# Optimization experiments

Hardware: AMD Instinct MI355X
Metric: run time of the kernel (lower is better)

## Reference

```python
import jax, jax.numpy as jnp
import numpy as np

ROPE_BASE = 10000.0
NUM_HEADS = 16

def _rotate_half(x):
    d = x.shape[-1] // 2
    return jnp.concatenate([-x[..., d:], x[..., :d]], axis=-1)

def setup_inputs() -> dict:
    key = jax.random.key(0)
    ks = jax.random.split(key, 5)
    b, s, d = 1, 2048, 2048
    scale = 1.0 / np.sqrt(d)
    return {
        "hidden_states": jax.random.normal(ks[0], (b, s, d), jnp.float32),
        "wq": jax.random.normal(ks[1], (d, d), jnp.float32) * scale,
        "wk": jax.random.normal(ks[2], (d, d), jnp.float32) * scale,
        "wv": jax.random.normal(ks[3], (d, d), jnp.float32) * scale,
        "wo": jax.random.normal(ks[4], (d, d), jnp.float32) * scale,
        "position_ids": jnp.broadcast_to(jnp.arange(s, dtype=jnp.int32), (b, s)),
    }

def reference(hidden_states, wq, wk, wv, wo, position_ids):
    b, s, d = hidden_states.shape
    h = NUM_HEADS
    dh = d // h
    # q/k/v projections (torch Linear: y = x @ W^T), split heads -> bhsd
    def proj(w):
        return jnp.einsum('bsd,ed->bse', hidden_states, w).reshape(b, s, h, dh).transpose(0, 2, 1, 3)
    q, k, v = proj(wq), proj(wk), proj(wv)
    # rotary embedding (LLaMA style): freqs over half dim, duplicated
    inv_freq = 1.0 / (ROPE_BASE ** (jnp.arange(0, dh, 2, dtype=jnp.float32) / dh))
    t = jnp.arange(s, dtype=jnp.float32)
    freqs = jnp.einsum('s,f->sf', t, inv_freq)              # [s, dh/2]
    emb = jnp.concatenate([freqs, freqs], axis=-1)          # [s, dh]
    cos = jnp.cos(emb)[position_ids][:, None, :, :]         # [b,1,s,dh]
    sin = jnp.sin(emb)[position_ids][:, None, :, :]
    q = q * cos + _rotate_half(q) * sin
    k = k * cos + _rotate_half(k) * sin
    # full (non-causal) scaled dot-product attention, as in the SDPA fast path
    scores = jnp.einsum('bhqd,bhkd->bhqk', q, k) / jnp.sqrt(jnp.float32(dh))
    attn = jax.nn.softmax(scores, axis=-1)
    out = jnp.einsum('bhqk,bhkd->bhqd', attn, v)            # [b,h,s,dh]
    out = out.transpose(0, 2, 1, 3).reshape(b, s, d)
    return jnp.einsum('bsd,ed->bse', out, wo)
```

## Files before the change

### kernel.cpp

```cpp
#include <hip/hip_runtime.h>

typedef unsigned short ushort_t;
typedef unsigned int uint32;
typedef __attribute__((ext_vector_type(8))) short short8;
typedef __attribute__((ext_vector_type(4))) float f32x4;
typedef __attribute__((ext_vector_type(2))) uint32 u32x2;

#define LDS_LOAD16(gptr, lptr)                                                             \
  __builtin_amdgcn_global_load_lds((const __attribute__((address_space(1))) uint32*)(gptr),\
                                   (__attribute__((address_space(3))) uint32*)(lptr),      \
                                   16, 0, 0)

__device__ __forceinline__ ushort_t f2b(float f) {
  uint32 u = __builtin_bit_cast(uint32, f);
  u += 0x7fffu + ((u >> 16) & 1u);
  return (ushort_t)(u >> 16);
}
__device__ __forceinline__ uint32 pk2(float a, float b) {
  return (uint32)f2b(a) | ((uint32)f2b(b) << 16);
}
__device__ __forceinline__ int swz8(int r) { return (r ^ (r >> 3)) & 7; }

constexpr size_t E = (size_t)2048 * 2048;

__global__ __launch_bounds__(256) void k_cvt5(const float* __restrict__ a0, const float* __restrict__ a1,
                                              const float* __restrict__ a2, const float* __restrict__ a3,
                                              const float* __restrict__ a4, ushort_t* __restrict__ out) {
  const float* srcs[5] = {a0, a1, a2, a3, a4};
  const float* s = srcs[blockIdx.y];
  size_t i = ((size_t)blockIdx.x * 256 + threadIdx.x) * 4;
  float4 v = *(const float4*)(s + i);
  ushort4 o;
  o.x = f2b(v.x); o.y = f2b(v.y); o.z = f2b(v.z); o.w = f2b(v.w);
  *(ushort4*)(out + (size_t)blockIdx.y * E + i) = o;
}

__global__ __launch_bounds__(256) void k_gemm_qkv(const ushort_t* __restrict__ A,
                                                  const ushort_t* __restrict__ B0,
                                                  const ushort_t* __restrict__ B1,
                                                  const ushort_t* __restrict__ B2,
                                                  ushort_t* __restrict__ Qm,
                                                  ushort_t* __restrict__ Km,
                                                  ushort_t* __restrict__ Vt,
                                                  const int* __restrict__ pos) {
  __shared__ ushort_t As[128 * 64];
  __shared__ ushort_t Bs[128 * 64];
  const int tid = threadIdx.x;
  const int lane = tid & 63, wave = tid >> 6;
  const int quad = lane >> 4, l16 = lane & 15;
  const int wm = wave >> 1, wn = wave & 1;
  const int z = blockIdx.z;
  const ushort_t* Bp = (z == 0) ? B0 : (z == 1) ? B1 : B2;
  const size_t row0 = (size_t)blockIdx.y * 128, col0 = (size_t)blockIdx.x * 128;

  int g[4];
#pragma unroll
  for (int j = 0; j < 4; ++j) g[j] = (j & 1) + ((j >> 1) << 2) + wn * 2;

  f32x4 zero = {0.f, 0.f, 0.f, 0.f};
  f32x4 acc[4][4];
#pragma unroll
  for (int i = 0; i < 4; ++i)
#pragma unroll
    for (int j = 0; j < 4; ++j) acc[i][j] = zero;

  for (int kt = 0; kt < 32; ++kt) {
#pragma unroll
    for (int j2 = 0; j2 < 4; ++j2) {
      int c = tid + 256 * j2;
      int r = c >> 3, p = c & 7;
      int sc = (p ^ swz8(r)) * 8;
      LDS_LOAD16(A + (row0 + r) * 2048 + kt * 64 + sc, &As[c * 8]);
      LDS_LOAD16(Bp + (col0 + r) * 2048 + kt * 64 + sc, &Bs[c * 8]);
    }
    __syncthreads();
    short8 a[4][2], b[4][2];
#pragma unroll
    for (int i = 0; i < 4; ++i) {
      int ra = wm * 64 + i * 16 + l16;
#pragma unroll
      for (int kk = 0; kk < 2; ++kk)
        a[i][kk] = *(const short8*)&As[(ra * 8 + ((kk * 4 + quad) ^ swz8(ra))) * 8];
    }
#pragma unroll
    for (int j = 0; j < 4; ++j) {
      int rb = g[j] * 16 + l16;
#pragma unroll
      for (int kk = 0; kk < 2; ++kk)
        b[j][kk] = *(const short8*)&Bs[(rb * 8 + ((kk * 4 + quad) ^ swz8(rb))) * 8];
    }
#pragma unroll
    for (int kk = 0; kk < 2; ++kk)
#pragma unroll
      for (int i = 0; i < 4; ++i)
#pragma unroll
        for (int j = 0; j < 4; ++j)
          acc[i][j] = __builtin_amdgcn_mfma_f32_16x16x32_bf16(a[i][kk], b[j][kk], acc[i][j], 0, 0, 0);
    __syncthreads();
  }

  if (z < 2) {
    ushort_t* C = z ? Km : Qm;
    const float mul = z ? 1.0f : 0.08838834764831845f;
#pragma unroll
    for (int i = 0; i < 4; ++i)
#pragma unroll
      for (int r = 0; r < 4; ++r) {
        size_t row = row0 + wm * 64 + i * 16 + quad * 4 + r;
        float pt = (float)pos[row];
        size_t rowoff = row * 2048 + col0;
#pragma unroll
        for (int j = 0; j < 2; ++j) {
          int f = g[j] * 16 + l16;
          float ang = pt * __expf(-0.14391156831212787f * (float)f);
          float sn, cs;
          __sincosf(ang, &sn, &cs);
          cs *= mul; sn *= mul;
          float q0 = acc[i][j][r], q1 = acc[i][j + 2][r];
          C[rowoff + f]      = f2b(q0 * cs - q1 * sn);
          C[rowoff + f + 64] = f2b(q1 * cs + q0 * sn);
        }
      }
  } else {
#pragma unroll
    for (int i = 0; i < 4; ++i)
#pragma unroll
      for (int j = 0; j < 4; ++j) {
        size_t col = col0 + g[j] * 16 + l16;
        size_t rowb = row0 + wm * 64 + i * 16 + quad * 4;
        ushort4 ov;
        ov.x = f2b(acc[i][j][0]); ov.y = f2b(acc[i][j][1]);
        ov.z = f2b(acc[i][j][2]); ov.w = f2b(acc[i][j][3]);
        *(ushort4*)&Vt[col * 2048 + rowb] = ov;
      }
  }
}

__global__ __launch_bounds__(256, 2) void k_attn(const ushort_t* __restrict__ Q,
                                                 const ushort_t* __restrict__ Kg,
                                                 const ushort_t* __restrict__ Vt,
                                                 ushort_t* __restrict__ O) {
  __shared__ uint32 smem[9216 + 256];
  ushort_t* Qs  = (ushort_t*)smem;
  uint32*   Pbf = smem + 4096;
  float*    Lred = (float*)(smem + 9216);
  float*    Rbuf = (float*)smem;

  const int tid = threadIdx.x;
  const int lane = tid & 63, wave = tid >> 6;
  const int quad = lane >> 4, l16 = lane & 15;
  const int bid = blockIdx.x;
  const int head = ((bid & 7) << 1) + ((bid >> 3) >> 5);
  const int qt = (bid >> 3) & 31;

#pragma unroll
  for (int j = 0; j < 4; ++j) {
    int s = tid + 256 * j;
    int r = s >> 4, p = s & 15;
    LDS_LOAD16(Q + (size_t)(qt * 64 + r) * 2048 + head * 128 + ((p ^ (r & 15)) * 8), &Qs[s * 8]);
  }
  __syncthreads();

  f32x4 zero = {0.f, 0.f, 0.f, 0.f};
  f32x4 oacc[4][8];
#pragma unroll
  for (int qg = 0; qg < 4; ++qg)
#pragma unroll
    for (int ns = 0; ns < 8; ++ns) oacc[qg][ns] = zero;
  float l_acc[4] = {0.f, 0.f, 0.f, 0.f};

  const ushort_t* Kbase = Kg + (size_t)head * 128;
  const ushort_t* Vbase = Vt + (size_t)head * 128 * 2048;
  uint32* pw = Pbf + wave * 1280;

  for (int it = 0; it < 16; ++it) {
    const int kb = it * 128 + wave * 32;

    short8 kf[2][4];
#pragma unroll
    for (int kg = 0; kg < 2; ++kg)
#pragma unroll
      for (int kk = 0; kk < 4; ++kk)
        kf[kg][kk] = *(const short8*)&Kbase[(size_t)(kb + kg * 16 + l16) * 2048 + kk * 32 + quad * 8];

#pragma unroll
    for (int qg = 0; qg < 4; ++qg) {
      short8 qa[4];
#pragma unroll
      for (int kk = 0; kk < 4; ++kk)
        qa[kk] = *(const short8*)&Qs[((qg * 16 + l16) * 16 + ((kk * 4 + quad) ^ l16)) * 8];
      f32x4 s0 = zero, s1 = zero;
#pragma unroll
      for (int kk = 0; kk < 4; ++kk) {
        s0 = __builtin_amdgcn_mfma_f32_16x16x32_bf16(kf[0][kk], qa[kk], s0, 0, 0, 0);
        s1 = __builtin_amdgcn_mfma_f32_16x16x32_bf16(kf[1][kk], qa[kk], s1, 0, 0, 0);
      }
      float p00 = __expf(s0[0]), p01 = __expf(s0[1]);
      float p02 = __expf(s0[2]), p03 = __expf(s0[3]);
      float p10 = __expf(s1[0]), p11 = __expf(s1[1]);
      float p12 = __expf(s1[2]), p13 = __expf(s1[3]);
      l_acc[qg] += ((p00 + p01) + (p02 + p03)) + ((p10 + p11) + (p12 + p13));
      u32x2 w0, w1;
      w0[0] = pk2(p00, p01); w0[1] = pk2(p02, p03);
      w1[0] = pk2(p10, p11); w1[1] = pk2(p12, p13);
      int off = (qg * 16 + l16) * 20 + quad * 2;
      *(u32x2*)&pw[off]     = w0;
      *(u32x2*)&pw[off + 8] = w1;
    }

    short8 pb[4];
#pragma unroll
    for (int qg = 0; qg < 4; ++qg)
      pb[qg] = *(const short8*)&pw[(qg * 16 + l16) * 20 + quad * 4];

#pragma unroll
    for (int ns = 0; ns < 8; ++ns) {
      const short8 vf = *(const short8*)&Vbase[(size_t)(ns * 16 + l16) * 2048 + kb + quad * 8];
#pragma unroll
      for (int qg = 0; qg < 4; ++qg)
        oacc[qg][ns] = __builtin_amdgcn_mfma_f32_16x16x32_bf16(vf, pb[qg], oacc[qg][ns], 0, 0, 0);
    }
  }

#pragma unroll
  for (int qg = 0; qg < 4; ++qg) {
    float l = l_acc[qg];
    l += __shfl_xor(l, 16, 64);
    l += __shfl_xor(l, 32, 64);
    l_acc[qg] = l;
  }
  if (quad == 0) {
#pragma unroll
    for (int qg = 0; qg < 4; ++qg) Lred[wave * 64 + qg * 16 + l16] = l_acc[qg];
  }

  const int tq = tid >> 4;
  const int td = (tid & 15) * 8;
  for (int qg = 0; qg < 4; ++qg) {
    __syncthreads();
#pragma unroll
    for (int ns = 0; ns < 8; ++ns)
      *(f32x4*)&Rbuf[(wave * 16 + l16) * 132 + ns * 16 + quad * 4] = oacc[qg][ns];
    __syncthreads();
    float lt = Lred[qg * 16 + tq] + Lred[64 + qg * 16 + tq] +
               Lred[128 + qg * 16 + tq] + Lred[192 + qg * 16 + tq];
    float inv = 1.0f / lt;
    f32x4 sA = zero, sB = zero;
#pragma unroll
    for (int w = 0; w < 4; ++w) {
      sA += *(const f32x4*)&Rbuf[(w * 16 + tq) * 132 + td];
      sB += *(const f32x4*)&Rbuf[(w * 16 + tq) * 132 + td + 4];
    }
    ushort4 o1, o2;
    o1.x = f2b(sA[0] * inv); o1.y = f2b(sA[1] * inv);
    o1.z = f2b(sA[2] * inv); o1.w = f2b(sA[3] * inv);
    o2.x = f2b(sB[0] * inv); o2.y = f2b(sB[1] * inv);
    o2.z = f2b(sB[2] * inv); o2.w = f2b(sB[3] * inv);
    size_t orow = (size_t)(qt * 64 + qg * 16 + tq) * 2048 + head * 128 + td;
    *(ushort4*)&O[orow] = o1;
    *(ushort4*)&O[orow + 4] = o2;
  }
}

__global__ __launch_bounds__(256) void k_gemm_wo_sk(const ushort_t* __restrict__ A,
                                                    const ushort_t* __restrict__ B,
                                                    float* __restrict__ P) {
  __shared__ ushort_t As[128 * 64];
  __shared__ ushort_t Bs[128 * 64];
  const int tid = threadIdx.x;
  const int lane = tid & 63, wave = tid >> 6;
  const int quad = lane >> 4, l16 = lane & 15;
  const int wm = wave >> 1, wn = wave & 1;
  const size_t row0 = (size_t)blockIdx.y * 128, col0 = (size_t)blockIdx.x * 128;
  const int k0 = blockIdx.z * 1024;
  float* Pz = P + (size_t)blockIdx.z * E;

  f32x4 zero = {0.f, 0.f, 0.f, 0.f};
  f32x4 acc[4][4];
#pragma unroll
  for (int i = 0; i < 4; ++i)
#pragma unroll
    for (int j = 0; j < 4; ++j) acc[i][j] = zero;

  for (int kt = 0; kt < 16; ++kt) {
#pragma unroll
    for (int j2 = 0; j2 < 4; ++j2) {
      int c = tid + 256 * j2;
      int r = c >> 3, p = c & 7;
      int sc = (p ^ swz8(r)) * 8;
      LDS_LOAD16(A + (row0 + r) * 2048 + k0 + kt * 64 + sc, &As[c * 8]);
      LDS_LOAD16(B + (col0 + r) * 2048 + k0 + kt * 64 + sc, &Bs[c * 8]);
    }
    __syncthreads();
    short8 a[4][2], b[4][2];
#pragma unroll
    for (int i = 0; i < 4; ++i) {
      int ra = wm * 64 + i * 16 + l16;
#pragma unroll
      for (int kk = 0; kk < 2; ++kk)
        a[i][kk] = *(const short8*)&As[(ra * 8 + ((kk * 4 + quad) ^ swz8(ra))) * 8];
    }
#pragma unroll
    for (int j = 0; j < 4; ++j) {
      int rb = wn * 64 + j * 16 + l16;
#pragma unroll
      for (int kk = 0; kk < 2; ++kk)
        b[j][kk] = *(const short8*)&Bs[(rb * 8 + ((kk * 4 + quad) ^ swz8(rb))) * 8];
    }
#pragma unroll
    for (int kk = 0; kk < 2; ++kk)
#pragma unroll
      for (int i = 0; i < 4; ++i)
#pragma unroll
        for (int j = 0; j < 4; ++j)
          acc[i][j] = __builtin_amdgcn_mfma_f32_16x16x32_bf16(a[i][kk], b[j][kk], acc[i][j], 0, 0, 0);
    __syncthreads();
  }

#pragma unroll
  for (int i = 0; i < 4; ++i)
#pragma unroll
    for (int j = 0; j < 4; ++j)
#pragma unroll
      for (int r = 0; r < 4; ++r) {
        size_t row = row0 + wm * 64 + i * 16 + quad * 4 + r;
        size_t col = col0 + wn * 64 + j * 16 + l16;
        Pz[row * 2048 + col] = acc[i][j][r];
      }
}

__global__ __launch_bounds__(256) void k_red(const float* __restrict__ P, float* __restrict__ out) {
  size_t i = ((size_t)blockIdx.x * 256 + threadIdx.x) * 4;
  f32x4 a = *(const f32x4*)(P + i);
  f32x4 b = *(const f32x4*)(P + E + i);
  *(f32x4*)(out + i) = a + b;
}

extern "C" void kernel_launch(void* const* d_in, const int* in_sizes, int n_in,
                              void* d_out, int out_size, void* d_ws, size_t ws_size,
                              hipStream_t stream) {
  const float* X  = (const float*)d_in[0];
  const float* wq = (const float*)d_in[1];
  const float* wk = (const float*)d_in[2];
  const float* wv = (const float*)d_in[3];
  const float* wo = (const float*)d_in[4];
  const int*  pos = (const int*)d_in[5];
  float* out = (float*)d_out;

  if (ws_size < 9 * E * sizeof(ushort_t)) return;

  ushort_t* Xb  = (ushort_t*)d_ws;
  ushort_t* Wqb = Xb + E;
  ushort_t* Wkb = Xb + 2 * E;
  ushort_t* Wvb = Xb + 3 * E;
  ushort_t* Wob = Xb + 4 * E;
  ushort_t* Qm  = Xb + 5 * E;
  ushort_t* Km  = Xb + 6 * E;
  ushort_t* Vtm = Xb + 7 * E;
  ushort_t* Om  = Xb + 8 * E;
  float* Pf = (float*)Xb;

  dim3 b256(256);
  k_cvt5<<<dim3(4096, 5), b256, 0, stream>>>(X, wq, wk, wv, wo, Xb);
  k_gemm_qkv<<<dim3(16, 16, 3), b256, 0, stream>>>(Xb, Wqb, Wkb, Wvb, Qm, Km, Vtm, pos);
  k_attn<<<512, b256, 0, stream>>>(Qm, Km, Vtm, Om);
  k_gemm_wo_sk<<<dim3(16, 16, 2), b256, 0, stream>>>(Om, Wob, Pf);
  k_red<<<4096, b256, 0, stream>>>(Pf, out);
}
```

Before: 317.7 us.

## Halve attention query tile to 32 rows, doubling blocks and raising occupancy

The attention kernel now processes 32 query rows per block instead of 64 and launches 1024 blocks instead of 512. Per-wave accumulators shrink from 4x8 to 2x8 MFMA tiles, and the LDS buffers are split and resized, which allows a launch bound of 3 blocks per SM. The aim is better CU fill and occupancy on a 256-CU part for latency hiding. In exchange, each K/V tile is reused across half as many queries, doubling total K/V global/L2 traffic, and the epilogue takes more barrier rounds.

```diff
diff --git a/kernel.cpp b/kernel.cpp
--- a/kernel.cpp
+++ b/kernel.cpp
@@ -136,42 +136,41 @@
   }
 }
 
-__global__ __launch_bounds__(256, 2) void k_attn(const ushort_t* __restrict__ Q,
+__global__ __launch_bounds__(256, 3) void k_attn(const ushort_t* __restrict__ Q,
                                                  const ushort_t* __restrict__ Kg,
                                                  const ushort_t* __restrict__ Vt,
                                                  ushort_t* __restrict__ O) {
-  __shared__ uint32 smem[9216 + 256];
-  ushort_t* Qs  = (ushort_t*)smem;
-  uint32*   Pbf = smem + 4096;
-  float*    Lred = (float*)(smem + 9216);
-  float*    Rbuf = (float*)smem;
+  __shared__ ushort_t Qs[32 * 128];
+  __shared__ uint32 Pbf[4 * 32 * 20];
+  __shared__ float Rbuf[4 * 16 * 68];
+  __shared__ float Lred[4][2][16];
 
   const int tid = threadIdx.x;
   const int lane = tid & 63, wave = tid >> 6;
   const int quad = lane >> 4, l16 = lane & 15;
   const int bid = blockIdx.x;
-  const int head = ((bid & 7) << 1) + ((bid >> 3) >> 5);
-  const int qt = (bid >> 3) & 31;
-
-#pragma unroll
-  for (int j = 0; j < 4; ++j) {
+  const int head = ((bid & 7) << 1) | (bid >> 9);
+  const int qt = (bid >> 3) & 63;
+
+#pragma unroll
+  for (int j = 0; j < 2; ++j) {
     int s = tid + 256 * j;
     int r = s >> 4, p = s & 15;
-    LDS_LOAD16(Q + (size_t)(qt * 64 + r) * 2048 + head * 128 + ((p ^ (r & 15)) * 8), &Qs[s * 8]);
+    LDS_LOAD16(Q + (size_t)(qt * 32 + r) * 2048 + head * 128 + ((p ^ (r & 15)) * 8), &Qs[s * 8]);
   }
   __syncthreads();
 
   f32x4 zero = {0.f, 0.f, 0.f, 0.f};
-  f32x4 oacc[4][8];
-#pragma unroll
-  for (int qg = 0; qg < 4; ++qg)
+  f32x4 oacc[2][8];
+#pragma unroll
+  for (int qg = 0; qg < 2; ++qg)
 #pragma unroll
     for (int ns = 0; ns < 8; ++ns) oacc[qg][ns] = zero;
-  float l_acc[4] = {0.f, 0.f, 0.f, 0.f};
+  float l_acc[2] = {0.f, 0.f};
 
   const ushort_t* Kbase = Kg + (size_t)head * 128;
   const ushort_t* Vbase = Vt + (size_t)head * 128 * 2048;
-  uint32* pw = Pbf + wave * 1280;
+  uint32* pw = Pbf + wave * 640;
 
   for (int it = 0; it < 16; ++it) {
     const int kb = it * 128 + wave * 32;
@@ -184,7 +183,7 @@
         kf[kg][kk] = *(const short8*)&Kbase[(size_t)(kb + kg * 16 + l16) * 2048 + kk * 32 + quad * 8];
 
 #pragma unroll
-    for (int qg = 0; qg < 4; ++qg) {
+    for (int qg = 0; qg < 2; ++qg) {
       short8 qa[4];
 #pragma unroll
       for (int kk = 0; kk < 4; ++kk)
@@ -208,58 +207,50 @@
       *(u32x2*)&pw[off + 8] = w1;
     }
 
-    short8 pb[4];
-#pragma unroll
-    for (int qg = 0; qg < 4; ++qg)
+    short8 pb[2];
+#pragma unroll
+    for (int qg = 0; qg < 2; ++qg)
       pb[qg] = *(const short8*)&pw[(qg * 16 + l16) * 20 + quad * 4];
 
 #pragma unroll
     for (int ns = 0; ns < 8; ++ns) {
       const short8 vf = *(const short8*)&Vbase[(size_t)(ns * 16 + l16) * 2048 + kb + quad * 8];
 #pragma unroll
-      for (int qg = 0; qg < 4; ++qg)
+      for (int qg = 0; qg < 2; ++qg)
         oacc[qg][ns] = __builtin_amdgcn_mfma_f32_16x16x32_bf16(vf, pb[qg], oacc[qg][ns], 0, 0, 0);
     }
   }
 
 #pragma unroll
-  for (int qg = 0; qg < 4; ++qg) {
+  for (int qg = 0; qg < 2; ++qg) {
     float l = l_acc[qg];
     l += __shfl_xor(l, 16, 64);
     l += __shfl_xor(l, 32, 64);
-    l_acc[qg] = l;
-  }
-  if (quad == 0) {
-#pragma unroll
-    for (int qg = 0; qg < 4; ++qg) Lred[wave * 64 + qg * 16 + l16] = l_acc[qg];
+    if (quad == 0) Lred[wave][qg][l16] = l;
   }
 
   const int tq = tid >> 4;
-  const int td = (tid & 15) * 8;
-  for (int qg = 0; qg < 4; ++qg) {
-    __syncthreads();
-#pragma unroll
-    for (int ns = 0; ns < 8; ++ns)
-      *(f32x4*)&Rbuf[(wave * 16 + l16) * 132 + ns * 16 + quad * 4] = oacc[qg][ns];
-    __syncthreads();
-    float lt = Lred[qg * 16 + tq] + Lred[64 + qg * 16 + tq] +
-               Lred[128 + qg * 16 + tq] + Lred[192 + qg * 16 + tq];
-    float inv = 1.0f / lt;
-    f32x4 sA = zero, sB = zero;
-#pragma unroll
-    for (int w = 0; w < 4; ++w) {
-      sA += *(const f32x4*)&Rbuf[(w * 16 + tq) * 132 + td];
-      sB += *(const f32x4*)&Rbuf[(w * 16 + tq) * 132 + td + 4];
-    }
-    ushort4 o1, o2;
-    o1.x = f2b(sA[0] * inv); o1.y = f2b(sA[1] * inv);
-    o1.z = f2b(sA[2] * inv); o1.w = f2b(sA[3] * inv);
-    o2.x = f2b(sB[0] * inv); o2.y = f2b(sB[1] * inv);
-    o2.z = f2b(sB[2] * inv); o2.w = f2b(sB[3] * inv);
-    size_t orow = (size_t)(qt * 64 + qg * 16 + tq) * 2048 + head * 128 + td;
-    *(ushort4*)&O[orow] = o1;
-    *(ushort4*)&O[orow + 4] = o2;
-  }
+  const int td4 = (tid & 15) * 4;
+#pragma unroll
+  for (int qg = 0; qg < 2; ++qg)
+#pragma unroll
+    for (int h = 0; h < 2; ++h) {
+      __syncthreads();
+#pragma unroll
+      for (int nl = 0; nl < 4; ++nl)
+        *(f32x4*)&Rbuf[(wave * 16 + l16) * 68 + nl * 16 + quad * 4] = oacc[qg][h * 4 + nl];
+      __syncthreads();
+      float lt = Lred[0][qg][tq] + Lred[1][qg][tq] + Lred[2][qg][tq] + Lred[3][qg][tq];
+      float inv = 1.0f / lt;
+      f32x4 sA = zero;
+#pragma unroll
+      for (int w = 0; w < 4; ++w) sA += *(const f32x4*)&Rbuf[(w * 16 + tq) * 68 + td4];
+      ushort4 o1;
+      o1.x = f2b(sA[0] * inv); o1.y = f2b(sA[1] * inv);
+      o1.z = f2b(sA[2] * inv); o1.w = f2b(sA[3] * inv);
+      size_t orow = (size_t)(qt * 32 + qg * 16 + tq) * 2048 + head * 128 + h * 64 + td4;
+      *(ushort4*)&O[orow] = o1;
+    }
 }
 
 __global__ __launch_bounds__(256) void k_gemm_wo_sk(const ushort_t* __restrict__ A,
@@ -363,7 +354,7 @@
   dim3 b256(256);
   k_cvt5<<<dim3(4096, 5), b256, 0, stream>>>(X, wq, wk, wv, wo, Xb);
   k_gemm_qkv<<<dim3(16, 16, 3), b256, 0, stream>>>(Xb, Wqb, Wkb, Wvb, Qm, Km, Vtm, pos);
-  k_attn<<<512, b256, 0, stream>>>(Qm, Km, Vtm, Om);
+  k_attn<<<1024, b256, 0, stream>>>(Qm, Km, Vtm, Om);
   k_gemm_wo_sk<<<dim3(16, 16, 2), b256, 0, stream>>>(Om, Wob, Pf);
   k_red<<<4096, b256, 0, stream>>>(Pf, out);
 }
```

After: 353.1 us. +11.2%, slower.
